# Optimization experiments

Hardware: AMD Instinct MI355X
Metric: run time of the kernel (lower is better)

Reference implementation:

```python
import jax, jax.numpy as jnp
import numpy as np

N_NODES = 100000
N_EDGES = 3200000
M = 24
HID = 32
OUT = 16


def neighbor_mean(feat, row, col, num_nodes):
    # sum features of source nodes into destination nodes, divide by in-degree
    sums = jax.ops.segment_sum(feat[row], col, num_segments=num_nodes)  # (N, F)
    deg = jax.ops.segment_sum(jnp.ones_like(col, dtype=feat.dtype), col, num_segments=num_nodes)
    return sums / jnp.clip(deg, 1.0)[:, None]


def sage_conv(x, row, col, num_nodes, w_l, b_l, w_r):
    # PyG SAGEConv(aggr='mean'): lin_l(mean_aggr) + lin_r(x); lin_r has no bias
    aggr = neighbor_mean(x, row, col, num_nodes)
    return aggr @ w_l.T + b_l + x @ w_r.T


def setup_inputs() -> dict:
    key = jax.random.key(0)
    ks = jax.random.split(key, 10)
    x_bin = jax.random.randint(ks[0], (N_NODES, M), 0, 2).astype(jnp.float32)
    edge_index = jax.random.randint(ks[1], (2, N_EDGES), 0, N_NODES).astype(jnp.int64)
    s = 0.1
    return {
        "x_bin": x_bin,
        "edge_index": edge_index,
        "w1l": s * jax.random.normal(ks[2], (HID, M), jnp.float32),
        "b1": s * jax.random.normal(ks[3], (HID,), jnp.float32),
        "w1r": s * jax.random.normal(ks[4], (HID, M), jnp.float32),
        "w2l": s * jax.random.normal(ks[5], (OUT, HID), jnp.float32),
        "b2": s * jax.random.normal(ks[6], (OUT,), jnp.float32),
        "w2r": s * jax.random.normal(ks[7], (OUT, HID), jnp.float32),
        "head_w": s * jax.random.normal(ks[8], (1, 3 * M + OUT), jnp.float32),
        "head_b": s * jax.random.normal(ks[9], (1,), jnp.float32),
    }


def reference(x_bin, edge_index, w1l, b1, w1r, w2l, b2, w2r, head_w, head_b):
    num_nodes = x_bin.shape[0]
    row, col = edge_index[0], edge_index[1]
    # explicit branch: [self markers | neighbor fraction | self * neighbor fraction]
    frac1 = neighbor_mean(x_bin, row, col, num_nodes)
    feats = jnp.concatenate([x_bin, frac1, x_bin * frac1], axis=1)  # (N, 3M)
    # GNN branch: SmallSAGE (dropout is identity at inference)
    h = jax.nn.relu(sage_conv(x_bin, row, col, num_nodes, w1l, b1, w1r))
    emb = jax.nn.relu(sage_conv(h, row, col, num_nodes, w2l, b2, w2r))  # (N, OUT)
    z = jnp.concatenate([feats, emb], axis=1)  # (N, 3M+OUT)
    yhat = (z @ head_w.T + head_b)[:, 0]  # (N,)
    return yhat, z
```

## Files before the change

kernel.cpp:

```cpp
#include <hip/hip_runtime.h>
#include <hip/hip_bf16.h>

#define MF 24
#define HIDF 32
#define OUTF 16
#define ZDIM 88
#define NPB 8
#define NPB2 32
#define SW1 28
#define SW2 36

#define NB 512
#define EB 4096
#define CAP 8192

union bf16x8 {
    float4 v;
    __hip_bfloat16 h[8];
};
union bf16x2u {
    unsigned int u;
    __hip_bfloat16 h[2];
};

__device__ __forceinline__ float ldw(const void* p, size_t i, bool bf16) {
    return bf16 ? __bfloat162float(((const __hip_bfloat16*)p)[i])
                : ((const float*)p)[i];
}

__device__ __forceinline__ bool detect_bf(const unsigned int* __restrict__ xw) {
    unsigned int w = xw[threadIdx.x & 63];
    return __ballot((w & 0xFFFFu) == 0x3F80u) != 0ull;
}
__device__ __forceinline__ bool detect_i64(const unsigned int* __restrict__ ew) {
    unsigned int w = ew[2 * (threadIdx.x & 63) + 1];
    return __popcll(__ballot(w == 0u)) >= 32;
}

__device__ __forceinline__ int bkt_of(int c, unsigned long long Wm) {
    return (int)(((unsigned long long)(unsigned)c * Wm) >> 32);
}

__device__ __forceinline__ float bf_lo(unsigned u) { return __uint_as_float(u << 16); }
__device__ __forceinline__ float bf_hi(unsigned u) { return __uint_as_float(u & 0xFFFF0000u); }

#define HIST_EDGE(c_)                                                   \
    if ((unsigned)(c_) < (unsigned)N) atomicAdd(&hist[bkt_of(c_, Wm)], 1);

__global__ __launch_bounds__(256) void k_histA(
    const void* __restrict__ x, unsigned int* __restrict__ xpack,
    const int* __restrict__ ei, int* __restrict__ counts,
    int nE, int N, unsigned long long Wm) {
    const bool bf16 = detect_bf((const unsigned int*)x);
    const bool i64 = detect_i64((const unsigned int*)ei);

    for (int n = blockIdx.x * 256 + threadIdx.x; n < N; n += gridDim.x * 256) {
        unsigned int m = 0;
        if (bf16) {
            const float4* xr = reinterpret_cast<const float4*>(
                (const __hip_bfloat16*)x + (size_t)n * MF);
            bf16x8 u;
#pragma unroll
            for (int q = 0; q < 3; ++q) {
                u.v = xr[q];
#pragma unroll
                for (int i = 0; i < 8; ++i)
                    if (__bfloat162float(u.h[i]) != 0.f) m |= 1u << (q * 8 + i);
            }
        } else {
            const float* xr = (const float*)x + (size_t)n * MF;
#pragma unroll
            for (int k = 0; k < MF; ++k)
                if (xr[k] != 0.f) m |= 1u << k;
        }
        xpack[n] = m;
    }

    __shared__ int hist[NB];
    for (int i = threadIdx.x; i < NB; i += 256) hist[i] = 0;
    __syncthreads();
    size_t base = (size_t)blockIdx.x * EB;
    int m = nE - (int)base;
    if (m > EB) m = EB;
    if (!(nE & 1)) {
        int nPair = m >> 1;
        if (i64) {
            const int4* cp = (const int4*)ei + (((size_t)nE + base) >> 1);
            for (int j = threadIdx.x; j < nPair; j += 256) {
                int4 c4 = cp[j];
                HIST_EDGE(c4.x);
                HIST_EDGE(c4.z);
            }
        } else {
            const int2* cp = (const int2*)ei + (((size_t)nE + base) >> 1);
            for (int j = threadIdx.x; j < nPair; j += 256) {
                int2 c2 = cp[j];
                HIST_EDGE(c2.x);
                HIST_EDGE(c2.y);
            }
        }
        for (int i = (nPair << 1) + threadIdx.x; i < m; i += 256) {
            size_t e = base + i;
            int c = i64 ? ei[2 * ((size_t)nE + e)] : ei[(size_t)nE + e];
            HIST_EDGE(c);
        }
    } else {
        for (int i = threadIdx.x; i < m; i += 256) {
            size_t e = base + i;
            int c = i64 ? ei[2 * ((size_t)nE + e)] : ei[(size_t)nE + e];
            HIST_EDGE(c);
        }
    }
    __syncthreads();
    for (int i = threadIdx.x; i < NB; i += 256)
        counts[(size_t)blockIdx.x * NB + i] = hist[i];
}

__global__ __launch_bounds__(1024) void k_colscan(int* __restrict__ counts,
                                                  int* __restrict__ colSum, int nBlk) {
    __shared__ int s[1024];
    int b = blockIdx.x, t = threadIdx.x;
    int v = (t < nBlk) ? counts[(size_t)t * NB + b] : 0;
    s[t] = v;
    __syncthreads();
    for (int off = 1; off < 1024; off <<= 1) {
        int y = (t >= off) ? s[t - off] : 0;
        __syncthreads();
        s[t] += y;
        __syncthreads();
    }
    if (t < nBlk) counts[(size_t)t * NB + b] = s[t] - v;
    if (t == 1023) colSum[b] = s[1023];
}

#define SCAT_EDGE(r_, c_)                                               \
    if ((unsigned)(c_) < (unsigned)N) {                                 \
        int b_ = bkt_of(c_, Wm);                                        \
        int ld_ = (c_) - b_ * W;                                        \
        unsigned rr_ = ((unsigned)(r_) < (unsigned)N) ? (unsigned)(r_) : 0u; \
        int pos_ = ldsStart[b_] + atomicAdd(&lcnt[b_], 1);              \
        rec[pos_] = rr_ | ((unsigned)ld_ << 20);                        \
        bkt[pos_] = (unsigned short)b_;                                 \
    }

__global__ __launch_bounds__(256) void k_scatB(
    const int* __restrict__ ei, const int* __restrict__ counts,
    const int* __restrict__ colSum,
    unsigned int* __restrict__ part, int nE, int N, int W,
    unsigned long long Wm, int nBlk) {
    const bool i64 = detect_i64((const unsigned int*)ei);
    __shared__ unsigned int rec[EB];
    __shared__ unsigned short bkt[EB];
    __shared__ int ldsStart[NB + 1];
    __shared__ int lcnt[NB];
    __shared__ int base2[NB];
    __shared__ int s256[256];
    const int t = threadIdx.x, blk = blockIdx.x;

    {
        int a0 = colSum[2 * t], a1 = colSum[2 * t + 1];
        int ps = a0 + a1;
        s256[t] = ps;
        __syncthreads();
        for (int off = 1; off < 256; off <<= 1) {
            int y = (t >= off) ? s256[t - off] : 0;
            __syncthreads();
            s256[t] += y;
            __syncthreads();
        }
        int base = s256[t] - ps;
        ldsStart[2 * t] = base;
        ldsStart[2 * t + 1] = base + a0;
        __syncthreads();
    }
    for (int b = t; b < NB; b += 256) {
        base2[b] = ldsStart[b] + counts[(size_t)blk * NB + b];
        lcnt[b] = 0;
    }
    __syncthreads();

    {
        int p0 = counts[(size_t)blk * NB + 2 * t];
        int p1 = counts[(size_t)blk * NB + 2 * t + 1];
        int n0 = (blk + 1 < nBlk) ? counts[(size_t)(blk + 1) * NB + 2 * t] : colSum[2 * t];
        int n1 = (blk + 1 < nBlk) ? counts[(size_t)(blk + 1) * NB + 2 * t + 1] : colSum[2 * t + 1];
        int v0 = n0 - p0, v1 = n1 - p1;
        int ps = v0 + v1;
        s256[t] = ps;
        __syncthreads();
        for (int off = 1; off < 256; off <<= 1) {
            int y = (t >= off) ? s256[t - off] : 0;
            __syncthreads();
            s256[t] += y;
            __syncthreads();
        }
        int base = s256[t] - ps;
        ldsStart[2 * t] = base;
        ldsStart[2 * t + 1] = base + v0;
        if (t == 255) ldsStart[NB] = base + ps;
        __syncthreads();
    }
    for (int b = t; b < NB; b += 256) base2[b] -= ldsStart[b];
    __syncthreads();

    size_t eb = (size_t)blk * EB;
    int m = nE - (int)eb;
    if (m > EB) m = EB;
    if (!(nE & 1)) {
        int nPair = m >> 1;
        if (i64) {
            const int4* rp = (const int4*)ei + (eb >> 1);
            const int4* cp = (const int4*)ei + (((size_t)nE + eb) >> 1);
            for (int j = t; j < nPair; j += 256) {
                int4 r4 = rp[j];
                int4 c4 = cp[j];
                SCAT_EDGE(r4.x, c4.x);
                SCAT_EDGE(r4.z, c4.z);
            }
        } else {
            const int2* rp = (const int2*)ei + (eb >> 1);
            const int2* cp = (const int2*)ei + (((size_t)nE + eb) >> 1);
            for (int j = t; j < nPair; j += 256) {
                int2 r2 = rp[j];
                int2 c2 = cp[j];
                SCAT_EDGE(r2.x, c2.x);
                SCAT_EDGE(r2.y, c2.y);
            }
        }
        for (int i = (nPair << 1) + t; i < m; i += 256) {
            size_t e = eb + i;
            int r = i64 ? ei[2 * e] : ei[e];
            int c = i64 ? ei[2 * ((size_t)nE + e)] : ei[(size_t)nE + e];
            SCAT_EDGE(r, c);
        }
    } else {
        for (int i = t; i < m; i += 256) {
            size_t e = eb + i;
            int r = i64 ? ei[2 * e] : ei[e];
            int c = i64 ? ei[2 * ((size_t)nE + e)] : ei[(size_t)nE + e];
            SCAT_EDGE(r, c);
        }
    }
    __syncthreads();

    int total = ldsStart[NB];
    for (int i = t; i < total; i += 256) {
        int b = bkt[i];
        part[base2[b] + i] = rec[i];
    }
}

__global__ __launch_bounds__(256) void k_csrC(const int* __restrict__ colSum,
                                              unsigned int* __restrict__ part,
                                              int* __restrict__ degi,
                                              int* __restrict__ rowstart,
                                              const unsigned int* __restrict__ xpack,
                                              unsigned int* __restrict__ cnt3,
                                              int N, int W) {
    __shared__ unsigned int stage[CAP];
    __shared__ unsigned long long c3[256 * 3];
    __shared__ int hist[256];
    __shared__ int sc[256];
    __shared__ int cur[256];
    int b = blockIdx.x, t = threadIdx.x;

    int p = ((t < b) ? colSum[t] : 0) + ((t + 256 < b) ? colSum[t + 256] : 0);
    sc[t] = p;
    __syncthreads();
    for (int off = 128; off > 0; off >>= 1) {
        if (t < off) sc[t] += sc[t + off];
        __syncthreads();
    }
    int start = sc[0];
    int bs = colSum[b];
    int node = b * W + t;

    hist[t] = 0;
#pragma unroll
    for (int j = 0; j < 3; ++j) c3[t * 3 + j] = 0ull;
    __syncthreads();

    if (bs > CAP) {
        if (t < W && node < N) {
            degi[node] = 0; rowstart[node] = start;
#pragma unroll
            for (int j = 0; j < 6; ++j) cnt3[(size_t)node * 6 + j] = 0;
        }
        return;
    }

    for (int i = t; i < bs; i += 256) {
        unsigned int v = part[start + i];
        stage[i] = v;
        int ld = v >> 20;
        atomicAdd(&hist[ld], 1);
        unsigned int xp = xpack[v & 0xFFFFFu];
        int b3 = ld * 3;
#pragma unroll
        for (int j = 0; j < 3; ++j) {
            unsigned int nlo = (xp >> (8 * j)) & 0xFu;
            unsigned int nhi = (xp >> (8 * j + 4)) & 0xFu;
            unsigned long long inc =
                (unsigned long long)((nlo * 0x00204081u) & 0x01010101u) |
                ((unsigned long long)((nhi * 0x00204081u) & 0x01010101u) << 32);
            atomicAdd(&c3[b3 + j], inc);
        }
    }
    __syncthreads();

    int v = hist[t];
    sc[t] = v;
    __syncthreads();
    for (int off = 1; off < 256; off <<= 1) {
        int y = (t >= off) ? sc[t - off] : 0;
        __syncthreads();
        sc[t] += y;
        __syncthreads();
    }
    int excl = sc[t] - v;
    if (t < W && node < N) {
        degi[node] = v;
        rowstart[node] = start + excl;
        const unsigned int* c3w = (const unsigned int*)c3;
#pragma unroll
        for (int j = 0; j < 6; ++j) cnt3[(size_t)node * 6 + j] = c3w[t * 6 + j];
    }
    cur[t] = excl;
    __syncthreads();

    for (int i = t; i < bs; i += 256) {
        unsigned int v2 = stage[i];
        int pos = atomicAdd(&cur[v2 >> 20], 1);
        part[start + pos] = v2 & 0xFFFFFu;
    }
}

__global__ __launch_bounds__(256) void k_layer1(
    const void* __restrict__ x, const unsigned int* __restrict__ xpack,
    const int* __restrict__ degi, const unsigned int* __restrict__ cnt3,
    void* __restrict__ out,
    const void* __restrict__ w1l, const void* __restrict__ b1,
    const void* __restrict__ w1r, const void* __restrict__ w2l,
    const void* __restrict__ b2, const void* __restrict__ w2r,
    const void* __restrict__ head_w,
    __hip_bfloat16* __restrict__ hl, __hip_bfloat16* __restrict__ st,
    float* __restrict__ ypart, int N) {
    const bool bf16 = detect_bf((const unsigned int*)x);
    __shared__ float swl[HIDF * SW1];
    __shared__ float swr[HIDF * SW1];
    __shared__ float sb[HIDF];
    __shared__ float s2l[OUTF * SW2];
    __shared__ float s2r[OUTF * SW2];
    __shared__ float sb2[OUTF];
    __shared__ float shw[3 * MF];
    __shared__ float fs[NPB][MF];
    __shared__ float hs[NPB][HIDF];
    const int t = threadIdx.x;

    if (bf16) {
        const uint4* al = (const uint4*)w1l;
        const uint4* ar = (const uint4*)w1r;
        if (t < 96) {
            uint4 vl = al[t], vr = ar[t];
            int i0 = t * 8;
            int j = i0 / MF, k = i0 - j * MF;
            float4 fl0 = make_float4(bf_lo(vl.x), bf_hi(vl.x), bf_lo(vl.y), bf_hi(vl.y));
            float4 fl1 = make_float4(bf_lo(vl.z), bf_hi(vl.z), bf_lo(vl.w), bf_hi(vl.w));
            float4 fr0 = make_float4(bf_lo(vr.x), bf_hi(vr.x), bf_lo(vr.y), bf_hi(vr.y));
            float4 fr1 = make_float4(bf_lo(vr.z), bf_hi(vr.z), bf_lo(vr.w), bf_hi(vr.w));
            float4* dl = (float4*)(swl + j * SW1 + k);
            float4* dr = (float4*)(swr + j * SW1 + k);
            dl[0] = fl0; dl[1] = fl1;
            dr[0] = fr0; dr[1] = fr1;
        }
        const uint4* bl = (const uint4*)w2l;
        const uint4* br = (const uint4*)w2r;
        if (t >= 128 && t < 192) {
            int c = t - 128;
            uint4 vl = bl[c], vr = br[c];
            int i0 = c * 8;
            int o = i0 >> 5, j = i0 & 31;
            float4 fl0 = make_float4(bf_lo(vl.x), bf_hi(vl.x), bf_lo(vl.y), bf_hi(vl.y));
            float4 fl1 = make_float4(bf_lo(vl.z), bf_hi(vl.z), bf_lo(vl.w), bf_hi(vl.w));
            float4 fr0 = make_float4(bf_lo(vr.x), bf_hi(vr.x), bf_lo(vr.y), bf_hi(vr.y));
            float4 fr1 = make_float4(bf_lo(vr.z), bf_hi(vr.z), bf_lo(vr.w), bf_hi(vr.w));
            float4* dl = (float4*)(s2l + o * SW2 + j);
            float4* dr = (float4*)(s2r + o * SW2 + j);
            dl[0] = fl0; dl[1] = fl1;
            dr[0] = fr0; dr[1] = fr1;
        }
    } else {
        const float4* al = (const float4*)w1l;
        const float4* ar = (const float4*)w1r;
        if (t < 192) {
            float4 vl = al[t], vr = ar[t];
            int i0 = t * 4;
            int j = i0 / MF, k = i0 - j * MF;
            *(float4*)(swl + j * SW1 + k) = vl;
            *(float4*)(swr + j * SW1 + k) = vr;
        }
        const float4* bl = (const float4*)w2l;
        const float4* br = (const float4*)w2r;
        int c = t - 128;
        if (c >= 0 && c < 128) {
            float4 vl = bl[c], vr = br[c];
            int i0 = c * 4;
            int o = i0 >> 5, j = i0 & 31;
            *(float4*)(s2l + o * SW2 + j) = vl;
            *(float4*)(s2r + o * SW2 + j) = vr;
        }
    }
    if (t < HIDF) sb[t] = ldw(b1, t, bf16);
    if (t >= 64 && t < 64 + OUTF) sb2[t - 64] = ldw(b2, t - 64, bf16);
    if (t >= 96 && t < 96 + 3 * MF) shw[t - 96] = ldw(head_w, t - 96, bf16);
    __syncthreads();

    const int lane = threadIdx.x & 31;
    const int wg = threadIdx.x >> 5;
    int node = blockIdx.x * NPB + wg;
    bool valid = node < N;

    int dg = 0;
    unsigned int xpn = 0;
    unsigned int cw = 0;
    if (valid) {
        dg = degi[node];
        xpn = xpack[node];
        if (lane < MF) cw = cnt3[(size_t)node * 6 + (lane >> 2)];
    }
    int cnt = (cw >> ((lane & 3) * 8)) & 0xFF;

    float inv = 1.f / fmaxf((float)dg, 1.f);
    float fv = (float)cnt * inv;
    float xv = (float)((xpn >> lane) & 1);

    float pc = 0.f;
    if (valid && lane < MF) {
        if (bf16) {
            __hip_bfloat16* z = (__hip_bfloat16*)out + N + (size_t)node * ZDIM;
            z[lane] = __float2bfloat16(xv);
            z[MF + lane] = __float2bfloat16(fv);
            z[2 * MF + lane] = __float2bfloat16(xv * fv);
        } else {
            float* z = (float*)out + N + (size_t)node * ZDIM;
            z[lane] = xv;
            z[MF + lane] = fv;
            z[2 * MF + lane] = xv * fv;
        }
        pc = xv * shw[lane] + fv * shw[MF + lane] + xv * fv * shw[2 * MF + lane];
    }

    if (lane < MF) fs[wg][lane] = fv;

    float fvk[MF];
    {
        const float4* fp = (const float4*)fs[wg];
#pragma unroll
        for (int q = 0; q < 6; ++q) {
            float4 f4 = fp[q];
            fvk[q * 4 + 0] = f4.x; fvk[q * 4 + 1] = f4.y;
            fvk[q * 4 + 2] = f4.z; fvk[q * 4 + 3] = f4.w;
        }
    }
    float wlv[MF], wrv[MF];
    {
        const float4* wl4 = (const float4*)(swl + lane * SW1);
        const float4* wr4 = (const float4*)(swr + lane * SW1);
#pragma unroll
        for (int q = 0; q < 6; ++q) {
            float4 a = wl4[q], b = wr4[q];
            wlv[q * 4 + 0] = a.x; wlv[q * 4 + 1] = a.y;
            wlv[q * 4 + 2] = a.z; wlv[q * 4 + 3] = a.w;
            wrv[q * 4 + 0] = b.x; wrv[q * 4 + 1] = b.y;
            wrv[q * 4 + 2] = b.z; wrv[q * 4 + 3] = b.w;
        }
    }
    float acc = sb[lane];
#pragma unroll
    for (int k = 0; k < MF; ++k) {
        acc = fmaf(fvk[k], wlv[k], acc);
        acc += ((xpn >> k) & 1u) ? wrv[k] : 0.f;
    }
    hs[wg][lane] = fmaxf(acc, 0.f);

#pragma unroll
    for (int off = 16; off > 0; off >>= 1) pc += __shfl_down(pc, off, 32);

    int o = lane & 15;
    int half = lane >> 4;
    const float4* wrow4 = (const float4*)((half ? s2r : s2l) + o * SW2);
    const float4* hp4 = (const float4*)hs[wg];
    float d = 0.f;
#pragma unroll
    for (int q = 0; q < 8; ++q) {
        float4 hq = hp4[q], wq = wrow4[q];
        d += hq.x * wq.x + hq.y * wq.y + hq.z * wq.z + hq.w * wq.w;
    }
    if (valid) {
        if (half == 0) hl[(size_t)node * OUTF + o] = __float2bfloat16(d);
        else st[(size_t)node * OUTF + o] = __float2bfloat16(d + sb2[o]);
        if (lane == 0) ypart[node] = pc;
    }
}

__global__ __launch_bounds__(256) void k_layer2(
    const void* __restrict__ x, const int* __restrict__ degi,
    const int* __restrict__ rowstart, const unsigned int* __restrict__ srcs,
    const __hip_bfloat16* __restrict__ hl, const __hip_bfloat16* __restrict__ st,
    const float* __restrict__ ypart, void* __restrict__ out,
    const void* __restrict__ head_w, const void* __restrict__ head_b, int N) {
    const bool bf16 = detect_bf((const unsigned int*)x);
    __shared__ float shw2[OUTF];
    __shared__ float shb;
    if (threadIdx.x < OUTF) shw2[threadIdx.x] = ldw(head_w, 3 * MF + threadIdx.x, bf16);
    if (threadIdx.x == 0) shb = ldw(head_b, 0, bf16);
    __syncthreads();

    int lane = threadIdx.x & 7;
    int g = threadIdx.x >> 3;
    int node = blockIdx.x * NPB2 + g;
    bool valid = node < N;

    int dg = 0, p0 = 0;
    if (valid) {
        dg = degi[node];
        p0 = rowstart[node];
    }
    const unsigned int* hlw = (const unsigned int*)hl;
    float s0 = 0.f, s1 = 0.f;
    int e = 0;
    for (; e + 8 <= dg; e += 8) {
        int i0 = srcs[p0 + e],     i1 = srcs[p0 + e + 1];
        int i2 = srcs[p0 + e + 2], i3 = srcs[p0 + e + 3];
        int i4 = srcs[p0 + e + 4], i5 = srcs[p0 + e + 5];
        int i6 = srcs[p0 + e + 6], i7 = srcs[p0 + e + 7];
        bf16x2u u0, u1, u2, u3, u4, u5, u6, u7;
        u0.u = hlw[(size_t)i0 * 8 + lane];
        u1.u = hlw[(size_t)i1 * 8 + lane];
        u2.u = hlw[(size_t)i2 * 8 + lane];
        u3.u = hlw[(size_t)i3 * 8 + lane];
        u4.u = hlw[(size_t)i4 * 8 + lane];
        u5.u = hlw[(size_t)i5 * 8 + lane];
        u6.u = hlw[(size_t)i6 * 8 + lane];
        u7.u = hlw[(size_t)i7 * 8 + lane];
        s0 += (__bfloat162float(u0.h[0]) + __bfloat162float(u1.h[0])) +
              (__bfloat162float(u2.h[0]) + __bfloat162float(u3.h[0])) +
              (__bfloat162float(u4.h[0]) + __bfloat162float(u5.h[0])) +
              (__bfloat162float(u6.h[0]) + __bfloat162float(u7.h[0]));
        s1 += (__bfloat162float(u0.h[1]) + __bfloat162float(u1.h[1])) +
              (__bfloat162float(u2.h[1]) + __bfloat162float(u3.h[1])) +
              (__bfloat162float(u4.h[1]) + __bfloat162float(u5.h[1])) +
              (__bfloat162float(u6.h[1]) + __bfloat162float(u7.h[1]));
    }
    for (; e + 4 <= dg; e += 4) {
        int a = srcs[p0 + e], b = srcs[p0 + e + 1];
        int c = srcs[p0 + e + 2], d = srcs[p0 + e + 3];
        bf16x2u ua, ub, uc, ud;
        ua.u = hlw[(size_t)a * 8 + lane];
        ub.u = hlw[(size_t)b * 8 + lane];
        uc.u = hlw[(size_t)c * 8 + lane];
        ud.u = hlw[(size_t)d * 8 + lane];
        s0 += (__bfloat162float(ua.h[0]) + __bfloat162float(ub.h[0])) +
              (__bfloat162float(uc.h[0]) + __bfloat162float(ud.h[0]));
        s1 += (__bfloat162float(ua.h[1]) + __bfloat162float(ub.h[1])) +
              (__bfloat162float(uc.h[1]) + __bfloat162float(ud.h[1]));
    }
    for (; e < dg; ++e) {
        bf16x2u ua;
        ua.u = hlw[(size_t)srcs[p0 + e] * 8 + lane];
        s0 += __bfloat162float(ua.h[0]);
        s1 += __bfloat162float(ua.h[1]);
    }

    float emb0 = 0.f, emb1 = 0.f;
    if (valid) {
        float inv = 1.f / fmaxf((float)dg, 1.f);
        bf16x2u us;
        us.u = ((const unsigned int*)st)[(size_t)node * 8 + lane];
        emb0 = fmaxf(s0 * inv + __bfloat162float(us.h[0]), 0.f);
        emb1 = fmaxf(s1 * inv + __bfloat162float(us.h[1]), 0.f);
        if (bf16) {
            bf16x2u up;
            up.h[0] = __float2bfloat16(emb0);
            up.h[1] = __float2bfloat16(emb1);
            unsigned int* zw = (unsigned int*)((__hip_bfloat16*)out + N +
                                               (size_t)node * ZDIM + 3 * MF);
            zw[lane] = up.u;
        } else {
            float2* zw = (float2*)((float*)out + N + (size_t)node * ZDIM + 3 * MF);
            zw[lane] = make_float2(emb0, emb1);
        }
    }
    float part = emb0 * shw2[2 * lane] + emb1 * shw2[2 * lane + 1];
#pragma unroll
    for (int off = 4; off > 0; off >>= 1) part += __shfl_down(part, off, 8);
    if (valid && lane == 0) {
        float y = ypart[node] + part + shb;
        if (bf16) ((__hip_bfloat16*)out)[node] = __float2bfloat16(y);
        else ((float*)out)[node] = y;
    }
}

extern "C" void kernel_launch(void* const* d_in, const int* in_sizes, int n_in,
                              void* d_out, int out_size, void* d_ws, size_t ws_size,
                              hipStream_t stream) {
    const void* x = d_in[0];
    const int* ei = (const int*)d_in[1];
    const void* w1l = d_in[2];
    const void* b1 = d_in[3];
    const void* w1r = d_in[4];
    const void* w2l = d_in[5];
    const void* b2 = d_in[6];
    const void* w2r = d_in[7];
    const void* head_w = d_in[8];
    const void* head_b = d_in[9];

    const int N = in_sizes[0] / MF;
    const int nE = in_sizes[1] / 2;
    const int W = (N + NB - 1) / NB;
    const unsigned long long Wm = (0x100000000ull / (unsigned)W) + 1;
    const int nBlkA = (nE + EB - 1) / EB;

    if (N > NB * 256 || N > 131072 || nBlkA > 1024 ||
        (size_t)nBlkA * NB < (size_t)N || nE < 64) return;

    int* colSum = (int*)((char*)d_ws + 256);
    int* degi = colSum + NB;
    int* rowstart = degi + N;
    int* counts = rowstart + N;
    unsigned int* part = (unsigned int*)(counts + (size_t)nBlkA * NB);
    unsigned int* xpack = part + nE;
    __hip_bfloat16* hl = (__hip_bfloat16*)(xpack + N);
    __hip_bfloat16* st = hl + (size_t)N * OUTF;
    unsigned int* cnt3 = (unsigned int*)(st + (size_t)N * OUTF);
    float* ypart = (float*)counts;

    const size_t need = 256 +
        ((size_t)NB + 2 * (size_t)N + (size_t)nBlkA * NB +
         (size_t)nE + (size_t)N + 6 * (size_t)N) * 4 + (size_t)N * OUTF * 2 * 2;
    if (ws_size < need) return;

    const int gb1 = (N + NPB - 1) / NPB;
    const int gb2 = (N + NPB2 - 1) / NPB2;
    k_histA<<<nBlkA, 256, 0, stream>>>(x, xpack, ei, counts, nE, N, Wm);
    k_colscan<<<NB, 1024, 0, stream>>>(counts, colSum, nBlkA);
    k_scatB<<<nBlkA, 256, 0, stream>>>(ei, counts, colSum,
                                       part, nE, N, W, Wm, nBlkA);
    k_csrC<<<NB, 256, 0, stream>>>(colSum, part, degi, rowstart,
                                   xpack, cnt3, N, W);
    k_layer1<<<gb1, 256, 0, stream>>>(x, xpack, degi, cnt3, d_out,
                                      w1l, b1, w1r, w2l, b2, w2r, head_w,
                                      hl, st, ypart, N);
    k_layer2<<<gb2, 256, 0, stream>>>(x, degi, rowstart, part, hl, st, ypart,
                                      d_out, head_w, head_b, N);
}
```

Baseline: 217.5 us.

## Drop per-node CSR sort; aggregate layer-2 via LDS atomics per bucket

The k_csrC pass no longer stages, scans and rewrites edges into per-node sorted order, and no longer writes rowstart. Instead a new k_aggr kernel walks each bucket's unsorted edges, loads 32-byte bf16 hidden rows, and accumulates them into a 256x17 shared-memory float array with atomics before applying mean, ReLU and the head. This removes a full rewrite pass over the edge array and the per-node gather kernel. In exchange it uses only 512 blocks, issues 16 LDS float atomics per edge, and makes the float summation order nondeterministic.

```diff
diff --git a/kernel.cpp b/kernel.cpp
--- a/kernel.cpp
+++ b/kernel.cpp
@@ -6,13 +6,11 @@
 #define OUTF 16
 #define ZDIM 88
 #define NPB 8
-#define NPB2 32
 #define SW1 28
 #define SW2 36
 
 #define NB 512
 #define EB 4096
-#define CAP 8192
 
 union bf16x8 {
     float4 v;
@@ -251,21 +249,21 @@
 }
 
 __global__ __launch_bounds__(256) void k_csrC(const int* __restrict__ colSum,
-                                              unsigned int* __restrict__ part,
+                                              const unsigned int* __restrict__ part,
                                               int* __restrict__ degi,
-                                              int* __restrict__ rowstart,
                                               const unsigned int* __restrict__ xpack,
                                               unsigned int* __restrict__ cnt3,
                                               int N, int W) {
-    __shared__ unsigned int stage[CAP];
     __shared__ unsigned long long c3[256 * 3];
     __shared__ int hist[256];
     __shared__ int sc[256];
-    __shared__ int cur[256];
     int b = blockIdx.x, t = threadIdx.x;
 
     int p = ((t < b) ? colSum[t] : 0) + ((t + 256 < b) ? colSum[t + 256] : 0);
     sc[t] = p;
+    hist[t] = 0;
+#pragma unroll
+    for (int j = 0; j < 3; ++j) c3[t * 3 + j] = 0ull;
     __syncthreads();
     for (int off = 128; off > 0; off >>= 1) {
         if (t < off) sc[t] += sc[t + off];
@@ -273,25 +271,9 @@
     }
     int start = sc[0];
     int bs = colSum[b];
-    int node = b * W + t;
-
-    hist[t] = 0;
-#pragma unroll
-    for (int j = 0; j < 3; ++j) c3[t * 3 + j] = 0ull;
-    __syncthreads();
-
-    if (bs > CAP) {
-        if (t < W && node < N) {
-            degi[node] = 0; rowstart[node] = start;
-#pragma unroll
-            for (int j = 0; j < 6; ++j) cnt3[(size_t)node * 6 + j] = 0;
-        }
-        return;
-    }
 
     for (int i = t; i < bs; i += 256) {
         unsigned int v = part[start + i];
-        stage[i] = v;
         int ld = v >> 20;
         atomicAdd(&hist[ld], 1);
         unsigned int xp = xpack[v & 0xFFFFFu];
@@ -308,30 +290,12 @@
     }
     __syncthreads();
 
-    int v = hist[t];
-    sc[t] = v;
-    __syncthreads();
-    for (int off = 1; off < 256; off <<= 1) {
-        int y = (t >= off) ? sc[t - off] : 0;
-        __syncthreads();
-        sc[t] += y;
-        __syncthreads();
-    }
-    int excl = sc[t] - v;
+    int node = b * W + t;
     if (t < W && node < N) {
-        degi[node] = v;
-        rowstart[node] = start + excl;
+        degi[node] = hist[t];
         const unsigned int* c3w = (const unsigned int*)c3;
 #pragma unroll
         for (int j = 0; j < 6; ++j) cnt3[(size_t)node * 6 + j] = c3w[t * 6 + j];
-    }
-    cur[t] = excl;
-    __syncthreads();
-
-    for (int i = t; i < bs; i += 256) {
-        unsigned int v2 = stage[i];
-        int pos = atomicAdd(&cur[v2 >> 20], 1);
-        part[start + pos] = v2 & 0xFFFFFu;
     }
 }
 
@@ -503,101 +467,91 @@
     }
 }
 
-__global__ __launch_bounds__(256) void k_layer2(
-    const void* __restrict__ x, const int* __restrict__ degi,
-    const int* __restrict__ rowstart, const unsigned int* __restrict__ srcs,
+__global__ __launch_bounds__(256) void k_aggr(
+    const void* __restrict__ x, const int* __restrict__ colSum,
+    const unsigned int* __restrict__ part, const int* __restrict__ degi,
     const __hip_bfloat16* __restrict__ hl, const __hip_bfloat16* __restrict__ st,
     const float* __restrict__ ypart, void* __restrict__ out,
-    const void* __restrict__ head_w, const void* __restrict__ head_b, int N) {
+    const void* __restrict__ head_w, const void* __restrict__ head_b,
+    int N, int W) {
     const bool bf16 = detect_bf((const unsigned int*)x);
+    __shared__ float acc[256][17];
+    __shared__ int sc[256];
     __shared__ float shw2[OUTF];
     __shared__ float shb;
-    if (threadIdx.x < OUTF) shw2[threadIdx.x] = ldw(head_w, 3 * MF + threadIdx.x, bf16);
-    if (threadIdx.x == 0) shb = ldw(head_b, 0, bf16);
-    __syncthreads();
-
-    int lane = threadIdx.x & 7;
-    int g = threadIdx.x >> 3;
-    int node = blockIdx.x * NPB2 + g;
-    bool valid = node < N;
-
-    int dg = 0, p0 = 0;
-    if (valid) {
-        dg = degi[node];
-        p0 = rowstart[node];
-    }
-    const unsigned int* hlw = (const unsigned int*)hl;
-    float s0 = 0.f, s1 = 0.f;
-    int e = 0;
-    for (; e + 8 <= dg; e += 8) {
-        int i0 = srcs[p0 + e],     i1 = srcs[p0 + e + 1];
-        int i2 = srcs[p0 + e + 2], i3 = srcs[p0 + e + 3];
-        int i4 = srcs[p0 + e + 4], i5 = srcs[p0 + e + 5];
-        int i6 = srcs[p0 + e + 6], i7 = srcs[p0 + e + 7];
-        bf16x2u u0, u1, u2, u3, u4, u5, u6, u7;
-        u0.u = hlw[(size_t)i0 * 8 + lane];
-        u1.u = hlw[(size_t)i1 * 8 + lane];
-        u2.u = hlw[(size_t)i2 * 8 + lane];
-        u3.u = hlw[(size_t)i3 * 8 + lane];
-        u4.u = hlw[(size_t)i4 * 8 + lane];
-        u5.u = hlw[(size_t)i5 * 8 + lane];
-        u6.u = hlw[(size_t)i6 * 8 + lane];
-        u7.u = hlw[(size_t)i7 * 8 + lane];
-        s0 += (__bfloat162float(u0.h[0]) + __bfloat162float(u1.h[0])) +
-              (__bfloat162float(u2.h[0]) + __bfloat162float(u3.h[0])) +
-              (__bfloat162float(u4.h[0]) + __bfloat162float(u5.h[0])) +
-              (__bfloat162float(u6.h[0]) + __bfloat162float(u7.h[0]));
-        s1 += (__bfloat162float(u0.h[1]) + __bfloat162float(u1.h[1])) +
-              (__bfloat162float(u2.h[1]) + __bfloat162float(u3.h[1])) +
-              (__bfloat162float(u4.h[1]) + __bfloat162float(u5.h[1])) +
-              (__bfloat162float(u6.h[1]) + __bfloat162float(u7.h[1]));
-    }
-    for (; e + 4 <= dg; e += 4) {
-        int a = srcs[p0 + e], b = srcs[p0 + e + 1];
-        int c = srcs[p0 + e + 2], d = srcs[p0 + e + 3];
-        bf16x2u ua, ub, uc, ud;
-        ua.u = hlw[(size_t)a * 8 + lane];
-        ub.u = hlw[(size_t)b * 8 + lane];
-        uc.u = hlw[(size_t)c * 8 + lane];
-        ud.u = hlw[(size_t)d * 8 + lane];
-        s0 += (__bfloat162float(ua.h[0]) + __bfloat162float(ub.h[0])) +
-              (__bfloat162float(uc.h[0]) + __bfloat162float(ud.h[0]));
-        s1 += (__bfloat162float(ua.h[1]) + __bfloat162float(ub.h[1])) +
-              (__bfloat162float(uc.h[1]) + __bfloat162float(ud.h[1]));
-    }
-    for (; e < dg; ++e) {
-        bf16x2u ua;
-        ua.u = hlw[(size_t)srcs[p0 + e] * 8 + lane];
-        s0 += __bfloat162float(ua.h[0]);
-        s1 += __bfloat162float(ua.h[1]);
-    }
-
-    float emb0 = 0.f, emb1 = 0.f;
-    if (valid) {
+    int b = blockIdx.x, t = threadIdx.x;
+
+    if (t < OUTF) shw2[t] = ldw(head_w, 3 * MF + t, bf16);
+    if (t == OUTF) shb = ldw(head_b, 0, bf16);
+
+    int p = ((t < b) ? colSum[t] : 0) + ((t + 256 < b) ? colSum[t + 256] : 0);
+    sc[t] = p;
+    {
+        float* af = &acc[0][0];
+        for (int j = t; j < 256 * 17; j += 256) af[j] = 0.f;
+    }
+    __syncthreads();
+    for (int off = 128; off > 0; off >>= 1) {
+        if (t < off) sc[t] += sc[t + off];
+        __syncthreads();
+    }
+    int start = sc[0];
+    int bs = colSum[b];
+
+    for (int i = t; i < bs; i += 256) {
+        unsigned int v = part[start + i];
+        int src = v & 0xFFFFF;
+        int ld = v >> 20;
+        const uint4* hp = (const uint4*)(hl + (size_t)src * OUTF);
+        uint4 a = hp[0], c = hp[1];
+        float* ar = acc[ld];
+        atomicAdd(&ar[0],  bf_lo(a.x)); atomicAdd(&ar[1],  bf_hi(a.x));
+        atomicAdd(&ar[2],  bf_lo(a.y)); atomicAdd(&ar[3],  bf_hi(a.y));
+        atomicAdd(&ar[4],  bf_lo(a.z)); atomicAdd(&ar[5],  bf_hi(a.z));
+        atomicAdd(&ar[6],  bf_lo(a.w)); atomicAdd(&ar[7],  bf_hi(a.w));
+        atomicAdd(&ar[8],  bf_lo(c.x)); atomicAdd(&ar[9],  bf_hi(c.x));
+        atomicAdd(&ar[10], bf_lo(c.y)); atomicAdd(&ar[11], bf_hi(c.y));
+        atomicAdd(&ar[12], bf_lo(c.z)); atomicAdd(&ar[13], bf_hi(c.z));
+        atomicAdd(&ar[14], bf_lo(c.w)); atomicAdd(&ar[15], bf_hi(c.w));
+    }
+    __syncthreads();
+
+    int node = b * W + t;
+    if (t < W && node < N) {
+        int dg = degi[node];
         float inv = 1.f / fmaxf((float)dg, 1.f);
-        bf16x2u us;
-        us.u = ((const unsigned int*)st)[(size_t)node * 8 + lane];
-        emb0 = fmaxf(s0 * inv + __bfloat162float(us.h[0]), 0.f);
-        emb1 = fmaxf(s1 * inv + __bfloat162float(us.h[1]), 0.f);
+        const unsigned int* sw = (const unsigned int*)st + (size_t)node * 8;
+        float pc2 = 0.f;
         if (bf16) {
-            bf16x2u up;
-            up.h[0] = __float2bfloat16(emb0);
-            up.h[1] = __float2bfloat16(emb1);
             unsigned int* zw = (unsigned int*)((__hip_bfloat16*)out + N +
                                                (size_t)node * ZDIM + 3 * MF);
-            zw[lane] = up.u;
+#pragma unroll
+            for (int j = 0; j < 8; ++j) {
+                unsigned int u = sw[j];
+                float e0 = fmaxf(acc[t][2 * j] * inv + bf_lo(u), 0.f);
+                float e1 = fmaxf(acc[t][2 * j + 1] * inv + bf_hi(u), 0.f);
+                bf16x2u up;
+                up.h[0] = __float2bfloat16(e0);
+                up.h[1] = __float2bfloat16(e1);
+                zw[j] = up.u;
+                pc2 += e0 * shw2[2 * j] + e1 * shw2[2 * j + 1];
+            }
+            float y = ypart[node] + pc2 + shb;
+            ((__hip_bfloat16*)out)[node] = __float2bfloat16(y);
         } else {
-            float2* zw = (float2*)((float*)out + N + (size_t)node * ZDIM + 3 * MF);
-            zw[lane] = make_float2(emb0, emb1);
-        }
-    }
-    float part = emb0 * shw2[2 * lane] + emb1 * shw2[2 * lane + 1];
-#pragma unroll
-    for (int off = 4; off > 0; off >>= 1) part += __shfl_down(part, off, 8);
-    if (valid && lane == 0) {
-        float y = ypart[node] + part + shb;
-        if (bf16) ((__hip_bfloat16*)out)[node] = __float2bfloat16(y);
-        else ((float*)out)[node] = y;
+            float* z = (float*)out + N + (size_t)node * ZDIM + 3 * MF;
+#pragma unroll
+            for (int j = 0; j < 8; ++j) {
+                unsigned int u = sw[j];
+                float e0 = fmaxf(acc[t][2 * j] * inv + bf_lo(u), 0.f);
+                float e1 = fmaxf(acc[t][2 * j + 1] * inv + bf_hi(u), 0.f);
+                z[2 * j] = e0;
+                z[2 * j + 1] = e1;
+                pc2 += e0 * shw2[2 * j] + e1 * shw2[2 * j + 1];
+            }
+            float y = ypart[node] + pc2 + shb;
+            ((float*)out)[node] = y;
+        }
     }
 }
 
@@ -626,31 +580,30 @@
 
     int* colSum = (int*)((char*)d_ws + 256);
     int* degi = colSum + NB;
-    int* rowstart = degi + N;
-    int* counts = rowstart + N;
+    int* counts = degi + N;
     unsigned int* part = (unsigned int*)(counts + (size_t)nBlkA * NB);
     unsigned int* xpack = part + nE;
-    __hip_bfloat16* hl = (__hip_bfloat16*)(xpack + N);
+    __hip_bfloat16* hl = (__hip_bfloat16*)(((uintptr_t)(xpack + N) + 31) &
+                                           ~(uintptr_t)31);
     __hip_bfloat16* st = hl + (size_t)N * OUTF;
     unsigned int* cnt3 = (unsigned int*)(st + (size_t)N * OUTF);
     float* ypart = (float*)counts;
 
     const size_t need = 256 +
-        ((size_t)NB + 2 * (size_t)N + (size_t)nBlkA * NB +
-         (size_t)nE + (size_t)N + 6 * (size_t)N) * 4 + (size_t)N * OUTF * 2 * 2;
+        ((size_t)NB + (size_t)N + (size_t)nBlkA * NB +
+         (size_t)nE + (size_t)N + 6 * (size_t)N) * 4 + 32 +
+        (size_t)N * OUTF * 2 * 2;
     if (ws_size < need) return;
 
     const int gb1 = (N + NPB - 1) / NPB;
-    const int gb2 = (N + NPB2 - 1) / NPB2;
     k_histA<<<nBlkA, 256, 0, stream>>>(x, xpack, ei, counts, nE, N, Wm);
     k_colscan<<<NB, 1024, 0, stream>>>(counts, colSum, nBlkA);
     k_scatB<<<nBlkA, 256, 0, stream>>>(ei, counts, colSum,
                                        part, nE, N, W, Wm, nBlkA);
-    k_csrC<<<NB, 256, 0, stream>>>(colSum, part, degi, rowstart,
-                                   xpack, cnt3, N, W);
+    k_csrC<<<NB, 256, 0, stream>>>(colSum, part, degi, xpack, cnt3, N, W);
     k_layer1<<<gb1, 256, 0, stream>>>(x, xpack, degi, cnt3, d_out,
                                       w1l, b1, w1r, w2l, b2, w2r, head_w,
                                       hl, st, ypart, N);
-    k_layer2<<<gb2, 256, 0, stream>>>(x, degi, rowstart, part, hl, st, ypart,
-                                      d_out, head_w, head_b, N);
-}
+    k_aggr<<<NB, 256, 0, stream>>>(x, colSum, part, degi, hl, st, ypart,
+                                   d_out, head_w, head_b, N, W);
+}
```

Result: slower. 440.4 us (+102.5%).
